# Kernel optimization log

Hardware: AMD Instinct MI355X
Metric: run time of the kernel (lower is better)

## Reference

```python
import jax, jax.numpy as jnp
import numpy as np

NUM_EXPERTS = 8
TOP_K = 2
N_EMBD = 1024
BLOCKING = 128
D_FFN = ((4 * N_EMBD // TOP_K) + BLOCKING - 1) // BLOCKING * BLOCKING  # 2048


def setup_inputs() -> dict:
    key = jax.random.key(0)
    k_x, k_r, k_w1, k_w2 = jax.random.split(key, 4)
    B, S = 4, 2048
    x = jax.random.normal(k_x, (B, S, N_EMBD), dtype=jnp.float32)
    # nn.Linear weight layout: [out_features, in_features]
    router_w = jax.random.normal(k_r, (NUM_EXPERTS, N_EMBD), dtype=jnp.float32) * 0.02
    # trunc_normal(std=0.02, a=-0.06, b=0.06) approximated by clipped normal
    w1 = jnp.clip(jax.random.normal(k_w1, (N_EMBD, NUM_EXPERTS * D_FFN), dtype=jnp.float32) * 0.02, -0.06, 0.06)
    w2 = jnp.clip(jax.random.normal(k_w2, (NUM_EXPERTS * D_FFN, N_EMBD), dtype=jnp.float32) * 0.02, -0.06, 0.06)
    return {"x": x, "router_w": router_w, "w1": w1, "w2": w2}


def reference(x, router_w, w1, w2):
    B, S, D = x.shape
    T = B * S
    x_flat = x.reshape(T, D)

    # Router
    router_logits = x_flat @ router_w.T                       # [T, E]
    router_probs = jax.nn.softmax(router_logits.astype(jnp.float32), axis=-1)
    expert_weights, selected_experts = jax.lax.top_k(router_probs, TOP_K)  # [T, K]
    expert_weights = expert_weights / expert_weights.sum(axis=-1, keepdims=True)
    expert_weights = expert_weights.astype(x.dtype)

    # Combine weights c[t, e] = sum_k weight[t, k] * [sel[t, k] == e]
    combine = jnp.zeros((T, NUM_EXPERTS), dtype=x.dtype)
    combine = combine.at[jnp.arange(T)[:, None], selected_experts].add(expert_weights)

    # Expert FFNs (math equivalent of block-sparse sdd/gelu/dsd + scatter-combine)
    w1r = w1.reshape(D, NUM_EXPERTS, D_FFN)
    w2r = w2.reshape(NUM_EXPERTS, D_FFN, D)
    out_flat = jnp.zeros((T, D), dtype=x.dtype)
    for e in range(NUM_EXPERTS):
        h = jax.nn.gelu(x_flat @ w1r[:, e, :], approximate=False)  # [T, d_ffn]
        out_flat = out_flat + combine[:, e:e + 1] * (h @ w2r[e])
    output = out_flat.reshape(B, S, D)

    # Aux losses
    router_z_loss = jnp.mean(jax.nn.logsumexp(router_logits, axis=-1) ** 2)
    p_i = router_probs.mean(axis=0)                           # [E]
    f_i = jnp.zeros((NUM_EXPERTS,), dtype=x.dtype).at[selected_experts.reshape(-1)].add(
        jnp.float32(1.0) / (T * TOP_K))
    load_balance_loss = NUM_EXPERTS * jnp.dot(f_i, p_i.astype(x.dtype))

    return output, router_z_loss, load_balance_loss, f_i
```

## Files before the change

### kernel.cpp

```cpp
#include <hip/hip_runtime.h>
#include <hip/hip_bf16.h>
#include <math.h>

#define T_TOK   8192
#define D_MODEL 1024
#define DFFN    2048
#define N_EXP   8
#define NASSIGN (T_TOK*2)

#define TM 256
#define BN 256
#define BK 64
#define TILE_MAX 72

#define WS_ZSUM     0
#define WS_PSUM     4
#define WS_COUNTS   64
#define WS_CURSOR   96
#define WS_OFFS     128
#define WS_NTILES   160
#define WS_TMAP     256
#define WS_SEL      4096
#define WS_WGT      69632
#define WS_AIDX     135168
#define WS_AW       200704
#define WS_XB       266240
#define WS_W1T      (WS_XB + 16777216)
#define WS_W2T      (WS_W1T + 33554432)
#define WS_H        (WS_W2T + 33554432)

typedef __attribute__((ext_vector_type(8))) short bf16x8;
typedef __attribute__((ext_vector_type(4))) float f32x4;
typedef __attribute__((ext_vector_type(4))) unsigned int u32x4;

static __device__ __forceinline__ unsigned short f2bf(float f) {
    unsigned int u = __builtin_bit_cast(unsigned int, f);
    u += 0x7fffu + ((u >> 16) & 1u);
    return (unsigned short)(u >> 16);
}

static __device__ __forceinline__ void gll16(const unsigned short* g, unsigned short* l) {
    __builtin_amdgcn_global_load_lds(
        (const __attribute__((address_space(1))) unsigned int*)g,
        (__attribute__((address_space(3))) unsigned int*)l, 16, 0, 0);
}

static __device__ __forceinline__ int frag_off(int row, int kc) {
    return (row * 8 + (kc ^ (row & 7))) * 8;
}

__global__ __launch_bounds__(256) void transpose_cvt_kernel(
    const float* __restrict__ in, unsigned short* __restrict__ out, int K, int N)
{
    int e = blockIdx.z;
    const float* inp = in + (size_t)e * K * N;
    unsigned short* outp = out + (size_t)e * K * N;
    __shared__ unsigned short tile[64][68];
    int k0 = blockIdx.y * 64, n0 = blockIdx.x * 64;
    int tid = threadIdx.x;
    int r = tid >> 4, c4 = (tid & 15) * 4;
    #pragma unroll
    for (int p = 0; p < 4; ++p) {
        int k = r + p * 16;
        float4 v = *(const float4*)(inp + (size_t)(k0 + k) * N + n0 + c4);
        tile[k][c4+0] = f2bf(v.x);
        tile[k][c4+1] = f2bf(v.y);
        tile[k][c4+2] = f2bf(v.z);
        tile[k][c4+3] = f2bf(v.w);
    }
    __syncthreads();
    int n = tid >> 2, kc = (tid & 3) * 16;
    unsigned short t[16];
    #pragma unroll
    for (int j = 0; j < 16; ++j) t[j] = tile[kc + j][n];
    unsigned short* o = outp + (size_t)(n0 + n) * K + k0 + kc;
    *(u32x4*)o       = *(u32x4*)t;
    *(u32x4*)(o + 8) = *(u32x4*)(t + 8);
}

__global__ __launch_bounds__(256) void router_kernel(
    const float* __restrict__ x, const float* __restrict__ rw,
    float* zsum, float* psum, int* counts, int* sel, float* wgt,
    unsigned short* __restrict__ xb)
{
    __shared__ float xs[32*129];
    __shared__ float rs[8*129];
    __shared__ float lg[32*9];
    __shared__ float blk_p[8];
    __shared__ int   blk_c[8];
    __shared__ float blk_z;
    int tid = threadIdx.x;
    if (tid < 8) { blk_p[tid] = 0.f; blk_c[tid] = 0; }
    if (tid == 8) blk_z = 0.f;
    int tb = blockIdx.x * 32;
    int tt = tid >> 3, e = tid & 7;
    float acc = 0.f;
    for (int c = 0; c < 8; ++c) {
        int c0 = c * 128;
        #pragma unroll
        for (int p = 0; p < 16; ++p) {
            int flat = p * 256 + tid;
            int r = flat >> 7, col = flat & 127;
            xs[r*129 + col] = x[(size_t)(tb + r)*D_MODEL + c0 + col];
        }
        #pragma unroll
        for (int p = 0; p < 4; ++p) {
            int flat = p * 256 + tid;
            int er = flat >> 7, col = flat & 127;
            rs[er*129 + col] = rw[(size_t)er*D_MODEL + c0 + col];
        }
        __syncthreads();
        {
            int rr = tid >> 3, cc = (tid & 7) * 16;
            unsigned short tmp[16];
            #pragma unroll
            for (int j = 0; j < 16; ++j) tmp[j] = f2bf(xs[rr*129 + cc + j]);
            unsigned short* o = xb + (size_t)(tb + rr)*D_MODEL + c0 + cc;
            *(u32x4*)o       = *(u32x4*)tmp;
            *(u32x4*)(o + 8) = *(u32x4*)(tmp + 8);
        }
        #pragma unroll 8
        for (int i = 0; i < 128; ++i)
            acc += xs[tt*129 + i] * rs[e*129 + i];
        __syncthreads();
    }
    lg[tt*9 + e] = acc;
    __syncthreads();
    if (tid < 32) {
        int t = tb + tid;
        float l[8], p[8];
        float mx = -1e30f;
        #pragma unroll
        for (int j = 0; j < 8; ++j) { l[j] = lg[tid*9 + j]; mx = fmaxf(mx, l[j]); }
        float se = 0.f;
        #pragma unroll
        for (int j = 0; j < 8; ++j) { p[j] = expf(l[j] - mx); se += p[j]; }
        float inv = 1.f / se;
        #pragma unroll
        for (int j = 0; j < 8; ++j) p[j] *= inv;
        float lse = mx + logf(se);
        atomicAdd(&blk_z, lse*lse);
        #pragma unroll
        for (int j = 0; j < 8; ++j) atomicAdd(&blk_p[j], p[j]);
        int i0 = 0; float b0 = p[0];
        #pragma unroll
        for (int j = 1; j < 8; ++j) if (p[j] > b0) { b0 = p[j]; i0 = j; }
        int i1 = -1; float b1 = -1.f;
        #pragma unroll
        for (int j = 0; j < 8; ++j) if (j != i0 && p[j] > b1) { b1 = p[j]; i1 = j; }
        float s = b0 + b1;
        sel[t*2+0] = i0; sel[t*2+1] = i1;
        wgt[t*2+0] = b0 / s; wgt[t*2+1] = b1 / s;
        atomicAdd(&blk_c[i0], 1); atomicAdd(&blk_c[i1], 1);
    }
    __syncthreads();
    if (tid < 8) {
        atomicAdd(&counts[tid], blk_c[tid]);
        unsafeAtomicAdd(&psum[tid], blk_p[tid]);
    }
    if (tid == 8) unsafeAtomicAdd(zsum, blk_z);
}

__global__ void finalize_kernel(const int* counts, const float* psum, const float* zsum,
                                int* offs, int* ntiles, int* tmap, float* out_tail)
{
    if (threadIdx.x != 0) return;
    int off = 0, nt = 0;
    float lb = 0.f;
    for (int e = 0; e < N_EXP; ++e) {
        int c = counts[e];
        offs[e] = off;
        for (int m0 = 0; m0 < c; m0 += TM) {
            tmap[nt*4+0] = e;
            tmap[nt*4+1] = off + m0;
            tmap[nt*4+2] = min(TM, c - m0);
            tmap[nt*4+3] = 0;
            nt++;
        }
        float fi = (float)c / (float)NASSIGN;
        out_tail[2 + e] = fi;
        lb += fi * (psum[e] / (float)T_TOK);
        off += c;
    }
    *ntiles = nt;
    out_tail[0] = zsum[0] / (float)T_TOK;
    out_tail[1] = (float)N_EXP * lb;
}

__global__ __launch_bounds__(256) void scatter_kernel(
    const int* __restrict__ sel, const float* __restrict__ wgt,
    const int* __restrict__ offs, int* cursor, int* aidx, float* aw)
{
    int t = blockIdx.x * 256 + threadIdx.x;
    if (t >= T_TOK) return;
    #pragma unroll
    for (int k = 0; k < 2; ++k) {
        int e = sel[t*2 + k];
        int pos = atomicAdd(&cursor[e], 1);
        int r = offs[e] + pos;
        aidx[r] = t;
        aw[r] = wgt[t*2 + k];
    }
}

__global__ __launch_bounds__(512, 2) void gemm1_kernel(
    const unsigned short* __restrict__ xb, const unsigned short* __restrict__ w1t,
    const int* __restrict__ aidx, const int* __restrict__ tmap,
    const int* __restrict__ ntiles, unsigned short* __restrict__ H)
{
    int bid = blockIdx.x;
    int xcd = bid & 7;
    int jj  = bid >> 3;
    int tile = (jj >> 3) * 8 + xcd;
    int n0   = (jj & 7) * BN;
    if (tile >= *ntiles) return;
    int e     = tmap[tile*4+0];
    int gr    = tmap[tile*4+1];
    int valid = tmap[tile*4+2];
    __shared__ unsigned short As[2][TM*BK];
    __shared__ unsigned short Bs[2][BN*BK];
    int tid = threadIdx.x;
    int lane = tid & 63, wave = tid >> 6;
    int wm = (wave >> 2) * 128, wn = (wave & 3) * 64;
    int q = lane >> 4, r16 = lane & 15;
    f32x4 acc[8][4];
    #pragma unroll
    for (int i = 0; i < 8; ++i)
        #pragma unroll
        for (int j = 0; j < 4; ++j) acc[i][j] = (f32x4){0.f, 0.f, 0.f, 0.f};

    const unsigned short* aga[4];
    const unsigned short* bga[4];
    int coff[4];
    #pragma unroll
    for (int u = 0; u < 4; ++u) {
        int cc = tid + u*512;
        int m = cc >> 3, kl = cc & 7;
        int kg = kl ^ (m & 7);
        int tok = aidx[gr + min(m, valid - 1)];
        aga[u] = xb + (size_t)tok * D_MODEL + kg*8;
        bga[u] = w1t + ((size_t)(e * DFFN + n0 + m)) * D_MODEL + kg*8;
        coff[u] = cc * 8;
    }

    const int NK = D_MODEL / BK;
    #pragma unroll
    for (int u = 0; u < 4; ++u) gll16(aga[u], &As[0][coff[u]]);
    #pragma unroll
    for (int u = 0; u < 4; ++u) gll16(bga[u], &Bs[0][coff[u]]);

    int cur = 0;
    for (int kt = 0; kt < NK; ++kt) {
        if (kt + 1 < NK) {
            int ko = (kt + 1) * BK;
            #pragma unroll
            for (int u = 0; u < 4; ++u) gll16(aga[u] + ko, &As[cur^1][coff[u]]);
            #pragma unroll
            for (int u = 0; u < 4; ++u) gll16(bga[u] + ko, &Bs[cur^1][coff[u]]);
            asm volatile("s_waitcnt vmcnt(8)" ::: "memory");
        } else {
            asm volatile("s_waitcnt vmcnt(0)" ::: "memory");
        }
        __builtin_amdgcn_sched_barrier(0);
        __builtin_amdgcn_s_barrier();
        asm volatile("" ::: "memory");
        const unsigned short* Ab = &As[cur][0];
        const unsigned short* Bb = &Bs[cur][0];
        __builtin_amdgcn_s_setprio(1);
        #pragma unroll
        for (int kh = 0; kh < 2; ++kh) {
            bf16x8 af[8], bfr[4];
            #pragma unroll
            for (int im = 0; im < 8; ++im)
                af[im] = *(const bf16x8*)&Ab[frag_off(wm + im*16 + r16, q + 4*kh)];
            #pragma unroll
            for (int in = 0; in < 4; ++in)
                bfr[in] = *(const bf16x8*)&Bb[frag_off(wn + in*16 + r16, q + 4*kh)];
            #pragma unroll
            for (int im = 0; im < 8; ++im)
                #pragma unroll
                for (int in = 0; in < 4; ++in)
                    acc[im][in] = __builtin_amdgcn_mfma_f32_16x16x32_bf16(af[im], bfr[in], acc[im][in], 0, 0, 0);
        }
        __builtin_amdgcn_s_setprio(0);
        asm volatile("" ::: "memory");
        __builtin_amdgcn_sched_barrier(0);
        __builtin_amdgcn_s_barrier();
        cur ^= 1;
    }
    #pragma unroll
    for (int im = 0; im < 8; ++im) {
        #pragma unroll
        for (int reg = 0; reg < 4; ++reg) {
            int m = wm + im*16 + q*4 + reg;
            if (m < valid) {
                size_t rowbase = (size_t)(gr + m) * DFFN + n0 + wn;
                #pragma unroll
                for (int in = 0; in < 4; ++in) {
                    float v = acc[im][in][reg];
                    float g = 0.5f * v * (1.0f + erff(v * 0.70710678118654752f));
                    H[rowbase + in*16 + r16] = f2bf(g);
                }
            }
        }
    }
}

__global__ __launch_bounds__(512, 2) void gemm2_kernel(
    const unsigned short* __restrict__ H, const unsigned short* __restrict__ w2t,
    const int* __restrict__ aidx, const float* __restrict__ aw,
    const int* __restrict__ tmap, const int* __restrict__ ntiles,
    float* __restrict__ out)
{
    int bid = blockIdx.x;
    int xcd = bid & 7;
    int jj  = bid >> 3;
    int tile = (jj >> 2) * 8 + xcd;
    int n0   = (jj & 3) * BN;
    if (tile >= *ntiles) return;
    int e     = tmap[tile*4+0];
    int gr    = tmap[tile*4+1];
    int valid = tmap[tile*4+2];
    __shared__ unsigned short As[2][TM*BK];
    __shared__ unsigned short Bs[2][BN*BK];
    int tid = threadIdx.x;
    int lane = tid & 63, wave = tid >> 6;
    int wm = (wave >> 2) * 128, wn = (wave & 3) * 64;
    int q = lane >> 4, r16 = lane & 15;
    f32x4 acc[8][4];
    #pragma unroll
    for (int i = 0; i < 8; ++i)
        #pragma unroll
        for (int j = 0; j < 4; ++j) acc[i][j] = (f32x4){0.f, 0.f, 0.f, 0.f};

    const unsigned short* aga[4];
    const unsigned short* bga[4];
    int coff[4];
    #pragma unroll
    for (int u = 0; u < 4; ++u) {
        int cc = tid + u*512;
        int m = cc >> 3, kl = cc & 7;
        int kg = kl ^ (m & 7);
        aga[u] = H + (size_t)(gr + min(m, valid - 1)) * DFFN + kg*8;
        bga[u] = w2t + (size_t)e * (DFFN * D_MODEL) + (size_t)(n0 + m) * DFFN + kg*8;
        coff[u] = cc * 8;
    }

    const int NK = DFFN / BK;
    #pragma unroll
    for (int u = 0; u < 4; ++u) gll16(aga[u], &As[0][coff[u]]);
    #pragma unroll
    for (int u = 0; u < 4; ++u) gll16(bga[u], &Bs[0][coff[u]]);

    int cur = 0;
    for (int kt = 0; kt < NK; ++kt) {
        if (kt + 1 < NK) {
            int ko = (kt + 1) * BK;
            #pragma unroll
            for (int u = 0; u < 4; ++u) gll16(aga[u] + ko, &As[cur^1][coff[u]]);
            #pragma unroll
            for (int u = 0; u < 4; ++u) gll16(bga[u] + ko, &Bs[cur^1][coff[u]]);
            asm volatile("s_waitcnt vmcnt(8)" ::: "memory");
        } else {
            asm volatile("s_waitcnt vmcnt(0)" ::: "memory");
        }
        __builtin_amdgcn_sched_barrier(0);
        __builtin_amdgcn_s_barrier();
        asm volatile("" ::: "memory");
        const unsigned short* Ab = &As[cur][0];
        const unsigned short* Bb = &Bs[cur][0];
        __builtin_amdgcn_s_setprio(1);
        #pragma unroll
        for (int kh = 0; kh < 2; ++kh) {
            bf16x8 af[8], bfr[4];
            #pragma unroll
            for (int im = 0; im < 8; ++im)
                af[im] = *(const bf16x8*)&Ab[frag_off(wm + im*16 + r16, q + 4*kh)];
            #pragma unroll
            for (int in = 0; in < 4; ++in)
                bfr[in] = *(const bf16x8*)&Bb[frag_off(wn + in*16 + r16, q + 4*kh)];
            #pragma unroll
            for (int im = 0; im < 8; ++im)
                #pragma unroll
                for (int in = 0; in < 4; ++in)
                    acc[im][in] = __builtin_amdgcn_mfma_f32_16x16x32_bf16(af[im], bfr[in], acc[im][in], 0, 0, 0);
        }
        __builtin_amdgcn_s_setprio(0);
        asm volatile("" ::: "memory");
        __builtin_amdgcn_sched_barrier(0);
        __builtin_amdgcn_s_barrier();
        cur ^= 1;
    }
    #pragma unroll
    for (int im = 0; im < 8; ++im) {
        #pragma unroll
        for (int reg = 0; reg < 4; ++reg) {
            int m = wm + im*16 + q*4 + reg;
            if (m < valid) {
                int t = aidx[gr + m];
                float w = aw[gr + m];
                float* orow = out + (size_t)t*D_MODEL + n0 + wn;
                #pragma unroll
                for (int in = 0; in < 4; ++in)
                    unsafeAtomicAdd(&orow[in*16 + r16], w * acc[im][in][reg]);
            }
        }
    }
}

extern "C" void kernel_launch(void* const* d_in, const int* in_sizes, int n_in,
                              void* d_out, int out_size, void* d_ws, size_t ws_size,
                              hipStream_t stream)
{
    const float* x  = (const float*)d_in[0];
    const float* rw = (const float*)d_in[1];
    const float* w1 = (const float*)d_in[2];
    const float* w2 = (const float*)d_in[3];
    float* out = (float*)d_out;
    char* ws = (char*)d_ws;
    float* zsum   = (float*)(ws + WS_ZSUM);
    float* psum   = (float*)(ws + WS_PSUM);
    int*   counts = (int*)(ws + WS_COUNTS);
    int*   cursor = (int*)(ws + WS_CURSOR);
    int*   offs   = (int*)(ws + WS_OFFS);
    int*   ntiles = (int*)(ws + WS_NTILES);
    int*   tmap   = (int*)(ws + WS_TMAP);
    int*   sel    = (int*)(ws + WS_SEL);
    float* wgt    = (float*)(ws + WS_WGT);
    int*   aidx   = (int*)(ws + WS_AIDX);
    float* aw     = (float*)(ws + WS_AW);
    unsigned short* xb  = (unsigned short*)(ws + WS_XB);
    unsigned short* w1t = (unsigned short*)(ws + WS_W1T);
    unsigned short* w2t = (unsigned short*)(ws + WS_W2T);
    unsigned short* H   = (unsigned short*)(ws + WS_H);

    hipMemsetAsync(d_out, 0, (size_t)T_TOK * D_MODEL * sizeof(float), stream);
    hipMemsetAsync(ws, 0, 256, stream);

    transpose_cvt_kernel<<<dim3(16384/64, 1024/64, 1), 256, 0, stream>>>(w1, w1t, 1024, 16384);
    transpose_cvt_kernel<<<dim3(1024/64, 2048/64, 8), 256, 0, stream>>>(w2, w2t, 2048, 1024);

    router_kernel<<<T_TOK/32, 256, 0, stream>>>(x, rw, zsum, psum, counts, sel, wgt, xb);
    finalize_kernel<<<1, 64, 0, stream>>>(counts, psum, zsum, offs, ntiles, tmap,
                                          out + (size_t)T_TOK * D_MODEL);
    scatter_kernel<<<T_TOK/256, 256, 0, stream>>>(sel, wgt, offs, cursor, aidx, aw);
    gemm1_kernel<<<dim3(TILE_MAX * (DFFN/BN)), 512, 0, stream>>>(xb, w1t, aidx, tmap, ntiles, H);
    gemm2_kernel<<<dim3(TILE_MAX * (D_MODEL/BN)), 512, 0, stream>>>(H, w2t, aidx, aw, tmap, ntiles, out);
}
```

Baseline: 601.9 us.

## Fuse expert GEMMs into persistent cooperative kernel with work queue and tile dependencies

```diff
diff --git a/kernel.cpp b/kernel.cpp
--- a/kernel.cpp
+++ b/kernel.cpp
@@ -19,12 +19,16 @@
 #define WS_CURSOR   96
 #define WS_OFFS     128
 #define WS_NTILES   160
-#define WS_TMAP     256
-#define WS_SEL      4096
-#define WS_WGT      69632
-#define WS_AIDX     135168
-#define WS_AW       200704
-#define WS_XB       266240
+#define WS_QHEAD    164
+#define WS_QTOTAL   168
+#define WS_DONE1    256
+#define WS_TMAP     1024
+#define WS_QITEMS   2560
+#define WS_SEL      8192
+#define WS_WGT      73728
+#define WS_AIDX     139264
+#define WS_AW       204800
+#define WS_XB       270336
 #define WS_W1T      (WS_XB + 16777216)
 #define WS_W2T      (WS_W1T + 33554432)
 #define WS_H        (WS_W2T + 33554432)
@@ -162,7 +166,8 @@
 }
 
 __global__ void finalize_kernel(const int* counts, const float* psum, const float* zsum,
-                                int* offs, int* ntiles, int* tmap, float* out_tail)
+                                int* offs, int* ntiles, int* tmap, int* qitems,
+                                int* qtotal, float* out_tail)
 {
     if (threadIdx.x != 0) return;
     int off = 0, nt = 0;
@@ -183,6 +188,14 @@
         off += c;
     }
     *ntiles = nt;
+    int q = 0;
+    for (int t = 0; t < nt; ++t)
+        for (int nb = 0; nb < DFFN/BN; ++nb)
+            qitems[q++] = (0 << 14) | (t << 4) | nb;
+    for (int t = 0; t < nt; ++t)
+        for (int nb = 0; nb < D_MODEL/BN; ++nb)
+            qitems[q++] = (1 << 14) | (t << 4) | nb;
+    *qtotal = q;
     out_tail[0] = zsum[0] / (float)T_TOK;
     out_tail[1] = (float)N_EXP * lb;
 }
@@ -203,23 +216,13 @@
     }
 }
 
-__global__ __launch_bounds__(512, 2) void gemm1_kernel(
+
+static __device__ __forceinline__ void gemm1_tile(
+    int e, int gr, int valid, int n0,
     const unsigned short* __restrict__ xb, const unsigned short* __restrict__ w1t,
-    const int* __restrict__ aidx, const int* __restrict__ tmap,
-    const int* __restrict__ ntiles, unsigned short* __restrict__ H)
-{
-    int bid = blockIdx.x;
-    int xcd = bid & 7;
-    int jj  = bid >> 3;
-    int tile = (jj >> 3) * 8 + xcd;
-    int n0   = (jj & 7) * BN;
-    if (tile >= *ntiles) return;
-    int e     = tmap[tile*4+0];
-    int gr    = tmap[tile*4+1];
-    int valid = tmap[tile*4+2];
-    __shared__ unsigned short As[2][TM*BK];
-    __shared__ unsigned short Bs[2][BN*BK];
-    int tid = threadIdx.x;
+    const int* __restrict__ aidx, unsigned short* __restrict__ H,
+    unsigned short (*As)[TM*BK], unsigned short (*Bs)[TM*BK], int tid)
+{
     int lane = tid & 63, wave = tid >> 6;
     int wm = (wave >> 2) * 128, wn = (wave & 3) * 64;
     int q = lane >> 4, r16 = lane & 15;
@@ -306,24 +309,13 @@
     }
 }
 
-__global__ __launch_bounds__(512, 2) void gemm2_kernel(
+static __device__ __forceinline__ void gemm2_tile(
+    int e, int gr, int valid, int n0,
     const unsigned short* __restrict__ H, const unsigned short* __restrict__ w2t,
     const int* __restrict__ aidx, const float* __restrict__ aw,
-    const int* __restrict__ tmap, const int* __restrict__ ntiles,
-    float* __restrict__ out)
-{
-    int bid = blockIdx.x;
-    int xcd = bid & 7;
-    int jj  = bid >> 3;
-    int tile = (jj >> 2) * 8 + xcd;
-    int n0   = (jj & 3) * BN;
-    if (tile >= *ntiles) return;
-    int e     = tmap[tile*4+0];
-    int gr    = tmap[tile*4+1];
-    int valid = tmap[tile*4+2];
-    __shared__ unsigned short As[2][TM*BK];
-    __shared__ unsigned short Bs[2][BN*BK];
-    int tid = threadIdx.x;
+    unsigned short (*As)[TM*BK], unsigned short (*Bs)[TM*BK],
+    float* __restrict__ out, int tid)
+{
     int lane = tid & 63, wave = tid >> 6;
     int wm = (wave >> 2) * 128, wn = (wave & 3) * 64;
     int q = lane >> 4, r16 = lane & 15;
@@ -406,6 +398,84 @@
             }
         }
     }
+}
+
+__global__ __launch_bounds__(512, 1) void moe_gemm_kernel(
+    const unsigned short* __restrict__ xb, const unsigned short* __restrict__ w1t,
+    const unsigned short* __restrict__ w2t, unsigned short* __restrict__ H,
+    const int* __restrict__ aidx, const float* __restrict__ aw,
+    const int* __restrict__ tmap, const int* __restrict__ qitems,
+    int* qhead, const int* qtotal, int* done1, float* __restrict__ out)
+{
+    __shared__ unsigned short As[2][TM*BK];
+    __shared__ unsigned short Bs[2][TM*BK];
+    __shared__ int s_item;
+    int tid = threadIdx.x;
+    int qt = *qtotal;
+    for (;;) {
+        __syncthreads();
+        if (tid == 0) s_item = atomicAdd(qhead, 1);
+        __syncthreads();
+        int it = s_item;
+        if (it >= qt) return;
+        int item = qitems[it];
+        int type = item >> 14;
+        int tile = (item >> 4) & 1023;
+        int nb   = item & 15;
+        int e     = tmap[tile*4+0];
+        int gr    = tmap[tile*4+1];
+        int valid = tmap[tile*4+2];
+        if (type == 0) {
+            gemm1_tile(e, gr, valid, nb * BN, xb, w1t, aidx, H, As, Bs, tid);
+            __threadfence();
+            __syncthreads();
+            if (tid == 0) atomicAdd(&done1[tile], 1);
+        } else {
+            if (tid == 0) {
+                while (__hip_atomic_load(done1 + tile, __ATOMIC_ACQUIRE,
+                                         __HIP_MEMORY_SCOPE_AGENT) < DFFN/BN)
+                    __builtin_amdgcn_s_sleep(8);
+            }
+            __syncthreads();
+            __threadfence();
+            gemm2_tile(e, gr, valid, nb * BN, H, w2t, aidx, aw, As, Bs, out, tid);
+        }
+    }
+}
+
+__global__ __launch_bounds__(512, 1) void gemm1_fb_kernel(
+    const unsigned short* __restrict__ xb, const unsigned short* __restrict__ w1t,
+    const int* __restrict__ aidx, const int* __restrict__ tmap,
+    const int* __restrict__ ntiles, unsigned short* __restrict__ H)
+{
+    int bid = blockIdx.x;
+    int xcd = bid & 7;
+    int jj  = bid >> 3;
+    int tile = (jj >> 3) * 8 + xcd;
+    int n0   = (jj & 7) * BN;
+    if (tile >= *ntiles) return;
+    __shared__ unsigned short As[2][TM*BK];
+    __shared__ unsigned short Bs[2][TM*BK];
+    gemm1_tile(tmap[tile*4+0], tmap[tile*4+1], tmap[tile*4+2], n0,
+               xb, w1t, aidx, H, As, Bs, threadIdx.x);
+}
+
+__global__ __launch_bounds__(512, 1) void gemm2_fb_kernel(
+    const unsigned short* __restrict__ H, const unsigned short* __restrict__ w2t,
+    const int* __restrict__ aidx, const float* __restrict__ aw,
+    const int* __restrict__ tmap, const int* __restrict__ ntiles,
+    float* __restrict__ out)
+{
+    int bid = blockIdx.x;
+    int xcd = bid & 7;
+    int jj  = bid >> 3;
+    int tile = (jj >> 2) * 8 + xcd;
+    int n0   = (jj & 3) * BN;
+    if (tile >= *ntiles) return;
+    __shared__ unsigned short As[2][TM*BK];
+    __shared__ unsigned short Bs[2][TM*BK];
+    gemm2_tile(tmap[tile*4+0], tmap[tile*4+1], tmap[tile*4+2], n0,
+               H, w2t, aidx, aw, As, Bs, out, threadIdx.x);
 }
 
 extern "C" void kernel_launch(void* const* d_in, const int* in_sizes, int n_in,
@@ -424,7 +494,11 @@
     int*   cursor = (int*)(ws + WS_CURSOR);
     int*   offs   = (int*)(ws + WS_OFFS);
     int*   ntiles = (int*)(ws + WS_NTILES);
+    int*   qhead  = (int*)(ws + WS_QHEAD);
+    int*   qtotal = (int*)(ws + WS_QTOTAL);
+    int*   done1  = (int*)(ws + WS_DONE1);
     int*   tmap   = (int*)(ws + WS_TMAP);
+    int*   qitems = (int*)(ws + WS_QITEMS);
     int*   sel    = (int*)(ws + WS_SEL);
     float* wgt    = (float*)(ws + WS_WGT);
     int*   aidx   = (int*)(ws + WS_AIDX);
@@ -435,15 +509,48 @@
     unsigned short* H   = (unsigned short*)(ws + WS_H);
 
     hipMemsetAsync(d_out, 0, (size_t)T_TOK * D_MODEL * sizeof(float), stream);
-    hipMemsetAsync(ws, 0, 256, stream);
+    hipMemsetAsync(ws, 0, 2560, stream);
 
     transpose_cvt_kernel<<<dim3(16384/64, 1024/64, 1), 256, 0, stream>>>(w1, w1t, 1024, 16384);
     transpose_cvt_kernel<<<dim3(1024/64, 2048/64, 8), 256, 0, stream>>>(w2, w2t, 2048, 1024);
 
     router_kernel<<<T_TOK/32, 256, 0, stream>>>(x, rw, zsum, psum, counts, sel, wgt, xb);
     finalize_kernel<<<1, 64, 0, stream>>>(counts, psum, zsum, offs, ntiles, tmap,
-                                          out + (size_t)T_TOK * D_MODEL);
+                                          qitems, qtotal, out + (size_t)T_TOK * D_MODEL);
     scatter_kernel<<<T_TOK/256, 256, 0, stream>>>(sel, wgt, offs, cursor, aidx, aw);
-    gemm1_kernel<<<dim3(TILE_MAX * (DFFN/BN)), 512, 0, stream>>>(xb, w1t, aidx, tmap, ntiles, H);
-    gemm2_kernel<<<dim3(TILE_MAX * (D_MODEL/BN)), 512, 0, stream>>>(H, w2t, aidx, aw, tmap, ntiles, out);
-}
+
+    static int coopGrid = -2;
+    if (coopGrid == -2) {
+        int nb = 0;
+        hipError_t oe = hipOccupancyMaxActiveBlocksPerMultiprocessor(
+            &nb, moe_gemm_kernel, 512, 0);
+        if (oe != hipSuccess || nb < 1) {
+            coopGrid = -1;
+        } else {
+            hipDeviceProp_t prop;
+            int cus = 256;
+            if (hipGetDeviceProperties(&prop, 0) == hipSuccess)
+                cus = prop.multiProcessorCount;
+            int cap = nb * cus;
+            coopGrid = cap < 256 ? cap : 256;
+            if (coopGrid < 1) coopGrid = -1;
+        }
+    }
+
+    bool launched = false;
+    if (coopGrid > 0) {
+        void* args[] = { (void*)&xb, (void*)&w1t, (void*)&w2t, (void*)&H,
+                         (void*)&aidx, (void*)&aw, (void*)&tmap, (void*)&qitems,
+                         (void*)&qhead, (void*)&qtotal, (void*)&done1, (void*)&out };
+        hipError_t le = hipLaunchCooperativeKernel(
+            (const void*)moe_gemm_kernel, dim3(coopGrid), dim3(512), args, 0, stream);
+        if (le == hipSuccess) launched = true;
+        else coopGrid = -1;
+    }
+    if (!launched) {
+        gemm1_fb_kernel<<<dim3(TILE_MAX * (DFFN/BN)), 512, 0, stream>>>(
+            xb, w1t, aidx, tmap, ntiles, H);
+        gemm2_fb_kernel<<<dim3(TILE_MAX * (D_MODEL/BN)), 512, 0, stream>>>(
+            H, w2t, aidx, aw, tmap, ntiles, out);
+    }
+}
```

After: 611.1 us. No clear change (+1.5%).

## Shrink GEMM tiles to 256x128x32, split-K gemm2, parallelize tile map build

Applied to the files above, without the earlier changes.

```diff
diff --git a/kernel.cpp b/kernel.cpp
--- a/kernel.cpp
+++ b/kernel.cpp
@@ -9,8 +9,8 @@
 #define NASSIGN (T_TOK*2)
 
 #define TM 256
-#define BN 256
-#define BK 64
+#define BN 128
+#define BK 32
 #define TILE_MAX 72
 
 #define WS_ZSUM     0
@@ -19,12 +19,12 @@
 #define WS_CURSOR   96
 #define WS_OFFS     128
 #define WS_NTILES   160
-#define WS_TMAP     256
-#define WS_SEL      4096
-#define WS_WGT      69632
-#define WS_AIDX     135168
-#define WS_AW       200704
-#define WS_XB       266240
+#define WS_TMAP     1024
+#define WS_SEL      8192
+#define WS_WGT      73728
+#define WS_AIDX     139264
+#define WS_AW       204800
+#define WS_XB       270336
 #define WS_W1T      (WS_XB + 16777216)
 #define WS_W2T      (WS_W1T + 33554432)
 #define WS_H        (WS_W2T + 33554432)
@@ -45,8 +45,8 @@
         (__attribute__((address_space(3))) unsigned int*)l, 16, 0, 0);
 }
 
-static __device__ __forceinline__ int frag_off(int row, int kc) {
-    return (row * 8 + (kc ^ (row & 7))) * 8;
+static __device__ __forceinline__ int fo32(int row, int kc) {
+    return (row * 4 + (kc ^ (row & 3))) * 8;
 }
 
 __global__ __launch_bounds__(256) void transpose_cvt_kernel(
@@ -164,27 +164,39 @@
 __global__ void finalize_kernel(const int* counts, const float* psum, const float* zsum,
                                 int* offs, int* ntiles, int* tmap, float* out_tail)
 {
-    if (threadIdx.x != 0) return;
-    int off = 0, nt = 0;
-    float lb = 0.f;
-    for (int e = 0; e < N_EXP; ++e) {
-        int c = counts[e];
-        offs[e] = off;
-        for (int m0 = 0; m0 < c; m0 += TM) {
-            tmap[nt*4+0] = e;
-            tmap[nt*4+1] = off + m0;
-            tmap[nt*4+2] = min(TM, c - m0);
-            tmap[nt*4+3] = 0;
-            nt++;
-        }
-        float fi = (float)c / (float)NASSIGN;
-        out_tail[2 + e] = fi;
-        lb += fi * (psum[e] / (float)T_TOK);
-        off += c;
-    }
-    *ntiles = nt;
-    out_tail[0] = zsum[0] / (float)T_TOK;
-    out_tail[1] = (float)N_EXP * lb;
+    __shared__ int s_base[9];
+    __shared__ int s_off[8];
+    __shared__ int s_cnt[8];
+    int tid = threadIdx.x;
+    if (tid == 0) {
+        int off = 0, nt = 0;
+        float lb = 0.f;
+        for (int e = 0; e < N_EXP; ++e) {
+            int c = counts[e];
+            offs[e] = off;
+            s_off[e] = off; s_cnt[e] = c; s_base[e] = nt;
+            nt += (c + TM - 1) / TM;
+            float fi = (float)c / (float)NASSIGN;
+            out_tail[2 + e] = fi;
+            lb += fi * (psum[e] / (float)T_TOK);
+            off += c;
+        }
+        s_base[8] = nt;
+        *ntiles = nt;
+        out_tail[0] = zsum[0] / (float)T_TOK;
+        out_tail[1] = (float)N_EXP * lb;
+    }
+    __syncthreads();
+    int nt = s_base[8];
+    for (int t = tid; t < nt; t += blockDim.x) {
+        int e = 0;
+        while (e < 7 && t >= s_base[e + 1]) ++e;
+        int i = t - s_base[e];
+        tmap[t*4+0] = e;
+        tmap[t*4+1] = s_off[e] + i * TM;
+        tmap[t*4+2] = min(TM, s_cnt[e] - i * TM);
+        tmap[t*4+3] = 0;
+    }
 }
 
 __global__ __launch_bounds__(256) void scatter_kernel(
@@ -203,7 +215,7 @@
     }
 }
 
-__global__ __launch_bounds__(512, 2) void gemm1_kernel(
+__global__ __launch_bounds__(256, 2) void gemm1_kernel(
     const unsigned short* __restrict__ xb, const unsigned short* __restrict__ w1t,
     const int* __restrict__ aidx, const int* __restrict__ tmap,
     const int* __restrict__ ntiles, unsigned short* __restrict__ H)
@@ -211,17 +223,18 @@
     int bid = blockIdx.x;
     int xcd = bid & 7;
     int jj  = bid >> 3;
-    int tile = (jj >> 3) * 8 + xcd;
-    int n0   = (jj & 7) * BN;
+    int nb  = jj & 15;
+    int tile = (jj >> 4) * 8 + xcd;
     if (tile >= *ntiles) return;
     int e     = tmap[tile*4+0];
     int gr    = tmap[tile*4+1];
     int valid = tmap[tile*4+2];
+    int n0 = nb * BN;
     __shared__ unsigned short As[2][TM*BK];
     __shared__ unsigned short Bs[2][BN*BK];
     int tid = threadIdx.x;
     int lane = tid & 63, wave = tid >> 6;
-    int wm = (wave >> 2) * 128, wn = (wave & 3) * 64;
+    int wm = (wave >> 1) * 128, wn = (wave & 1) * 64;
     int q = lane >> 4, r16 = lane & 15;
     f32x4 acc[8][4];
     #pragma unroll
@@ -229,35 +242,41 @@
         #pragma unroll
         for (int j = 0; j < 4; ++j) acc[i][j] = (f32x4){0.f, 0.f, 0.f, 0.f};
 
-    const unsigned short* aga[4];
-    const unsigned short* bga[4];
-    int coff[4];
+    const unsigned short* aga[4]; int acoff[4];
     #pragma unroll
     for (int u = 0; u < 4; ++u) {
-        int cc = tid + u*512;
-        int m = cc >> 3, kl = cc & 7;
-        int kg = kl ^ (m & 7);
-        int tok = aidx[gr + min(m, valid - 1)];
+        int c = tid + u*256;
+        int row = c >> 2, kl = c & 3;
+        int kg = kl ^ (row & 3);
+        int tok = aidx[gr + min(row, valid - 1)];
         aga[u] = xb + (size_t)tok * D_MODEL + kg*8;
-        bga[u] = w1t + ((size_t)(e * DFFN + n0 + m)) * D_MODEL + kg*8;
-        coff[u] = cc * 8;
+        acoff[u] = c * 8;
+    }
+    const unsigned short* bga[2]; int bcoff[2];
+    #pragma unroll
+    for (int u = 0; u < 2; ++u) {
+        int c = tid + u*256;
+        int row = c >> 2, kl = c & 3;
+        int kg = kl ^ (row & 3);
+        bga[u] = w1t + ((size_t)(e * DFFN + n0 + row)) * D_MODEL + kg*8;
+        bcoff[u] = c * 8;
     }
 
     const int NK = D_MODEL / BK;
     #pragma unroll
-    for (int u = 0; u < 4; ++u) gll16(aga[u], &As[0][coff[u]]);
-    #pragma unroll
-    for (int u = 0; u < 4; ++u) gll16(bga[u], &Bs[0][coff[u]]);
+    for (int u = 0; u < 4; ++u) gll16(aga[u], &As[0][acoff[u]]);
+    #pragma unroll
+    for (int u = 0; u < 2; ++u) gll16(bga[u], &Bs[0][bcoff[u]]);
 
     int cur = 0;
     for (int kt = 0; kt < NK; ++kt) {
         if (kt + 1 < NK) {
             int ko = (kt + 1) * BK;
             #pragma unroll
-            for (int u = 0; u < 4; ++u) gll16(aga[u] + ko, &As[cur^1][coff[u]]);
-            #pragma unroll
-            for (int u = 0; u < 4; ++u) gll16(bga[u] + ko, &Bs[cur^1][coff[u]]);
-            asm volatile("s_waitcnt vmcnt(8)" ::: "memory");
+            for (int u = 0; u < 4; ++u) gll16(aga[u] + ko, &As[cur^1][acoff[u]]);
+            #pragma unroll
+            for (int u = 0; u < 2; ++u) gll16(bga[u] + ko, &Bs[cur^1][bcoff[u]]);
+            asm volatile("s_waitcnt vmcnt(6)" ::: "memory");
         } else {
             asm volatile("s_waitcnt vmcnt(0)" ::: "memory");
         }
@@ -267,15 +286,14 @@
         const unsigned short* Ab = &As[cur][0];
         const unsigned short* Bb = &Bs[cur][0];
         __builtin_amdgcn_s_setprio(1);
-        #pragma unroll
-        for (int kh = 0; kh < 2; ++kh) {
+        {
             bf16x8 af[8], bfr[4];
             #pragma unroll
             for (int im = 0; im < 8; ++im)
-                af[im] = *(const bf16x8*)&Ab[frag_off(wm + im*16 + r16, q + 4*kh)];
+                af[im] = *(const bf16x8*)&Ab[fo32(wm + im*16 + r16, q)];
             #pragma unroll
             for (int in = 0; in < 4; ++in)
-                bfr[in] = *(const bf16x8*)&Bb[frag_off(wn + in*16 + r16, q + 4*kh)];
+                bfr[in] = *(const bf16x8*)&Bb[fo32(wn + in*16 + r16, q)];
             #pragma unroll
             for (int im = 0; im < 8; ++im)
                 #pragma unroll
@@ -306,7 +324,7 @@
     }
 }
 
-__global__ __launch_bounds__(512, 2) void gemm2_kernel(
+__global__ __launch_bounds__(256, 2) void gemm2_kernel(
     const unsigned short* __restrict__ H, const unsigned short* __restrict__ w2t,
     const int* __restrict__ aidx, const float* __restrict__ aw,
     const int* __restrict__ tmap, const int* __restrict__ ntiles,
@@ -315,17 +333,20 @@
     int bid = blockIdx.x;
     int xcd = bid & 7;
     int jj  = bid >> 3;
-    int tile = (jj >> 2) * 8 + xcd;
-    int n0   = (jj & 3) * BN;
+    int sub = jj & 15;
+    int tile = (jj >> 4) * 8 + xcd;
     if (tile >= *ntiles) return;
+    int nbk = sub & 7, kh = sub >> 3;
     int e     = tmap[tile*4+0];
     int gr    = tmap[tile*4+1];
     int valid = tmap[tile*4+2];
+    int n0 = nbk * BN;
+    int k0 = kh * 1024;
     __shared__ unsigned short As[2][TM*BK];
     __shared__ unsigned short Bs[2][BN*BK];
     int tid = threadIdx.x;
     int lane = tid & 63, wave = tid >> 6;
-    int wm = (wave >> 2) * 128, wn = (wave & 3) * 64;
+    int wm = (wave >> 1) * 128, wn = (wave & 1) * 64;
     int q = lane >> 4, r16 = lane & 15;
     f32x4 acc[8][4];
     #pragma unroll
@@ -333,34 +354,40 @@
         #pragma unroll
         for (int j = 0; j < 4; ++j) acc[i][j] = (f32x4){0.f, 0.f, 0.f, 0.f};
 
-    const unsigned short* aga[4];
-    const unsigned short* bga[4];
-    int coff[4];
+    const unsigned short* aga[4]; int acoff[4];
     #pragma unroll
     for (int u = 0; u < 4; ++u) {
-        int cc = tid + u*512;
-        int m = cc >> 3, kl = cc & 7;
-        int kg = kl ^ (m & 7);
-        aga[u] = H + (size_t)(gr + min(m, valid - 1)) * DFFN + kg*8;
-        bga[u] = w2t + (size_t)e * (DFFN * D_MODEL) + (size_t)(n0 + m) * DFFN + kg*8;
-        coff[u] = cc * 8;
-    }
-
-    const int NK = DFFN / BK;
-    #pragma unroll
-    for (int u = 0; u < 4; ++u) gll16(aga[u], &As[0][coff[u]]);
-    #pragma unroll
-    for (int u = 0; u < 4; ++u) gll16(bga[u], &Bs[0][coff[u]]);
+        int c = tid + u*256;
+        int row = c >> 2, kl = c & 3;
+        int kg = kl ^ (row & 3);
+        aga[u] = H + (size_t)(gr + min(row, valid - 1)) * DFFN + k0 + kg*8;
+        acoff[u] = c * 8;
+    }
+    const unsigned short* bga[2]; int bcoff[2];
+    #pragma unroll
+    for (int u = 0; u < 2; ++u) {
+        int c = tid + u*256;
+        int row = c >> 2, kl = c & 3;
+        int kg = kl ^ (row & 3);
+        bga[u] = w2t + (size_t)e * (DFFN * D_MODEL) + (size_t)(n0 + row) * DFFN + k0 + kg*8;
+        bcoff[u] = c * 8;
+    }
+
+    const int NK = 1024 / BK;
+    #pragma unroll
+    for (int u = 0; u < 4; ++u) gll16(aga[u], &As[0][acoff[u]]);
+    #pragma unroll
+    for (int u = 0; u < 2; ++u) gll16(bga[u], &Bs[0][bcoff[u]]);
 
     int cur = 0;
     for (int kt = 0; kt < NK; ++kt) {
         if (kt + 1 < NK) {
             int ko = (kt + 1) * BK;
             #pragma unroll
-            for (int u = 0; u < 4; ++u) gll16(aga[u] + ko, &As[cur^1][coff[u]]);
-            #pragma unroll
-            for (int u = 0; u < 4; ++u) gll16(bga[u] + ko, &Bs[cur^1][coff[u]]);
-            asm volatile("s_waitcnt vmcnt(8)" ::: "memory");
+            for (int u = 0; u < 4; ++u) gll16(aga[u] + ko, &As[cur^1][acoff[u]]);
+            #pragma unroll
+            for (int u = 0; u < 2; ++u) gll16(bga[u] + ko, &Bs[cur^1][bcoff[u]]);
+            asm volatile("s_waitcnt vmcnt(6)" ::: "memory");
         } else {
             asm volatile("s_waitcnt vmcnt(0)" ::: "memory");
         }
@@ -370,15 +397,14 @@
         const unsigned short* Ab = &As[cur][0];
         const unsigned short* Bb = &Bs[cur][0];
         __builtin_amdgcn_s_setprio(1);
-        #pragma unroll
-        for (int kh = 0; kh < 2; ++kh) {
+        {
             bf16x8 af[8], bfr[4];
             #pragma unroll
             for (int im = 0; im < 8; ++im)
-                af[im] = *(const bf16x8*)&Ab[frag_off(wm + im*16 + r16, q + 4*kh)];
+                af[im] = *(const bf16x8*)&Ab[fo32(wm + im*16 + r16, q)];
             #pragma unroll
             for (int in = 0; in < 4; ++in)
-                bfr[in] = *(const bf16x8*)&Bb[frag_off(wn + in*16 + r16, q + 4*kh)];
+                bfr[in] = *(const bf16x8*)&Bb[fo32(wn + in*16 + r16, q)];
             #pragma unroll
             for (int im = 0; im < 8; ++im)
                 #pragma unroll
@@ -441,9 +467,10 @@
     transpose_cvt_kernel<<<dim3(1024/64, 2048/64, 8), 256, 0, stream>>>(w2, w2t, 2048, 1024);
 
     router_kernel<<<T_TOK/32, 256, 0, stream>>>(x, rw, zsum, psum, counts, sel, wgt, xb);
-    finalize_kernel<<<1, 64, 0, stream>>>(counts, psum, zsum, offs, ntiles, tmap,
-                                          out + (size_t)T_TOK * D_MODEL);
+    finalize_kernel<<<1, 128, 0, stream>>>(counts, psum, zsum, offs, ntiles, tmap,
+                                           out + (size_t)T_TOK * D_MODEL);
     scatter_kernel<<<T_TOK/256, 256, 0, stream>>>(sel, wgt, offs, cursor, aidx, aw);
-    gemm1_kernel<<<dim3(TILE_MAX * (DFFN/BN)), 512, 0, stream>>>(xb, w1t, aidx, tmap, ntiles, H);
-    gemm2_kernel<<<dim3(TILE_MAX * (D_MODEL/BN)), 512, 0, stream>>>(H, w2t, aidx, aw, tmap, ntiles, out);
-}
+
+    gemm1_kernel<<<dim3(TILE_MAX * 16), 256, 0, stream>>>(xb, w1t, aidx, tmap, ntiles, H);
+    gemm2_kernel<<<dim3(TILE_MAX * 16), 256, 0, stream>>>(H, w2t, aidx, aw, tmap, ntiles, out);
+}
```

Measured after the change: 630.4 us. +4.7%, slower.
